# Kernel tuning notes

Hardware: AMD Instinct MI355X
Metric: run time of the kernel (lower is better)

## Reference

```python
import jax, jax.numpy as jnp
import numpy as np

P = 8192          # pool_size
D = 4096          # input_dim
B = 4             # batch
SPARSITY = 0.1
NC = int(P * P * SPARSITY)  # 6710886 COO nonzeros


def setup_inputs() -> dict:
    key = jax.random.key(0)
    ks = jax.random.split(key, 5)
    return {
        "x": jax.random.normal(ks[0], (B, D), dtype=jnp.float32),
        "W_proj": jax.random.normal(ks[1], (P, D), dtype=jnp.float32) / np.float32(np.sqrt(D)),
        "b_proj": jnp.zeros((P,), dtype=jnp.float32),
        "conn_values": jax.random.normal(ks[2], (NC,), dtype=jnp.float32) * 0.1,
        "sparse_state": jnp.zeros((P,), dtype=jnp.float32),
        "conn_rows": jax.random.randint(ks[3], (NC,), 0, P, dtype=jnp.int32),
        "conn_cols": jax.random.randint(ks[4], (NC,), 0, P, dtype=jnp.int32),
    }


def reference(x, W_proj, b_proj, conn_values, sparse_state, conn_rows, conn_cols):
    # input projection: [B, D] @ [D, P] -> [B, P]
    a = x @ W_proj.T + b_proj
    # quantile threshold over all elements of |a| (matches torch.quantile on full tensor)
    thr = jnp.quantile(jnp.abs(a), 1.0 - SPARSITY)
    mask = jnp.abs(a) > thr                     # [B, P]
    # decay old state, then overwrite active entries with row-0 activation
    a0, m0 = a[0], mask[0]                      # [P], [P]
    state = jnp.where(m0, a0, sparse_state * 0.9)
    # sparse COO matvec: recurrent[r] += v * state[c] for each nonzero (r, c, v)
    contrib = conn_values * state[conn_cols]    # [NC]
    recurrent = jax.ops.segment_sum(contrib, conn_rows, num_segments=P)
    # fused state update + exact GELU (torch nn.GELU default)
    new_state = jax.nn.gelu(state + 0.1 * recurrent, approximate=False)
    # BoundedAttractorState scalars
    active_count = m0.sum()
    mean_activity = jnp.where(
        active_count > 0,
        jnp.sum(jnp.where(m0, new_state, 0.0)) / jnp.maximum(active_count, 1).astype(new_state.dtype),
        0.0,
    )
    return new_state, active_count, mean_activity
```

## Files before the change

kernel.cpp:

```cpp
#include <hip/hip_runtime.h>
#include <math.h>

#define PP 8192
#define DD 4096
#define NTOT 32768
#define K_LOW 29490
#define NBINS 8192
#define SCALE 1048576.0f
#define INV_SCALE (1.0f / 1048576.0f)
#define MSCALE 262144.0f
#define INV_MSCALE (1.0f / 262144.0f)
#define LIST_CAP 3072

__device__ __forceinline__ float dot4(float4 w, float4 v) {
  return fmaf(w.x, v.x, fmaf(w.y, v.y, fmaf(w.z, v.z, w.w * v.w)));
}

__global__ __launch_bounds__(256, 4) void gemm_kernel(const float* __restrict__ x,
                                                      const float* __restrict__ W,
                                                      const float* __restrict__ bias,
                                                      float* __restrict__ a,
                                                      unsigned* __restrict__ hist,
                                                      int* __restrict__ rec,
                                                      int* __restrict__ acc) {
  if (blockIdx.x < 32) {
    hist[blockIdx.x * 256 + threadIdx.x] = 0u;
  } else if (blockIdx.x < 64) {
    rec[(blockIdx.x - 32) * 256 + threadIdx.x] = 0;
  } else if (blockIdx.x == 64 && threadIdx.x < 4) {
    acc[threadIdx.x] = 0;
  }
  const int wave = threadIdx.x >> 6;
  const int lane = threadIdx.x & 63;
  const int p0 = blockIdx.x * 8 + wave * 2;
  const float4* __restrict__ W0 = (const float4*)(W + (size_t)p0 * DD);
  const float4* __restrict__ W1 = W0 + (DD / 4);
  const float4* __restrict__ x4 = (const float4*)x;
  double a00 = 0.0, a01 = 0.0, a02 = 0.0, a03 = 0.0;
  double a10 = 0.0, a11 = 0.0, a12 = 0.0, a13 = 0.0;
  #pragma unroll 4
  for (int k = 0; k < 16; ++k) {
    const int i = lane + k * 64;
    float4 w0 = W0[i];
    float4 w1 = W1[i];
    float4 v0 = x4[i];
    float4 v1 = x4[1024 + i];
    float4 v2 = x4[2048 + i];
    float4 v3 = x4[3072 + i];
    a00 += (double)dot4(w0, v0);
    a01 += (double)dot4(w0, v1);
    a02 += (double)dot4(w0, v2);
    a03 += (double)dot4(w0, v3);
    a10 += (double)dot4(w1, v0);
    a11 += (double)dot4(w1, v1);
    a12 += (double)dot4(w1, v2);
    a13 += (double)dot4(w1, v3);
  }
  #pragma unroll
  for (int off = 32; off > 0; off >>= 1) {
    a00 += __shfl_down(a00, off);
    a01 += __shfl_down(a01, off);
    a02 += __shfl_down(a02, off);
    a03 += __shfl_down(a03, off);
    a10 += __shfl_down(a10, off);
    a11 += __shfl_down(a11, off);
    a12 += __shfl_down(a12, off);
    a13 += __shfl_down(a13, off);
  }
  if (lane == 0) {
    float b0 = bias[p0];
    float b1 = bias[p0 + 1];
    a[0 * PP + p0] = (float)a00 + b0;
    a[1 * PP + p0] = (float)a01 + b0;
    a[2 * PP + p0] = (float)a02 + b0;
    a[3 * PP + p0] = (float)a03 + b0;
    a[0 * PP + p0 + 1] = (float)a10 + b1;
    a[1 * PP + p0 + 1] = (float)a11 + b1;
    a[2 * PP + p0 + 1] = (float)a12 + b1;
    a[3 * PP + p0 + 1] = (float)a13 + b1;
  }
}

__global__ __launch_bounds__(1024) void hist_thr_kernel(const float* __restrict__ a,
                                                        unsigned* __restrict__ hist,
                                                        int* __restrict__ acc,
                                                        float* __restrict__ thr) {
  __shared__ union {
    unsigned h[NBINS];
    struct {
      unsigned scan[1024];
      unsigned list1[LIST_CAP];
      unsigned list2[LIST_CAP];
      unsigned n1, n2, b1, r1, b2, r2, vlo, vhi;
    } t;
  } sh;
  __shared__ int s_last;
  const int tid = threadIdx.x;

  #pragma unroll
  for (int j = 0; j < NBINS / 1024; ++j) sh.h[tid + j * 1024] = 0u;
  __syncthreads();
  const int base = blockIdx.x * 4096 + tid;
  #pragma unroll
  for (int k = 0; k < 4; ++k) {
    unsigned u = __float_as_uint(fabsf(a[base + k * 1024]));
    atomicAdd(&sh.h[u >> 18], 1u);
  }
  __syncthreads();
  #pragma unroll
  for (int j = 0; j < NBINS / 1024; ++j) {
    unsigned c = sh.h[tid + j * 1024];
    if (c) atomicAdd(&hist[tid + j * 1024], c);
  }

  __threadfence();
  __syncthreads();
  if (tid == 0) {
    unsigned d = atomicAdd((unsigned*)&acc[3], 1u);
    s_last = (d == 7u) ? 1 : 0;
  }
  __syncthreads();
  if (!s_last) return;
  __threadfence();

  const uint4* h4 = (const uint4*)hist;
  uint4 q0 = h4[tid * 2];
  uint4 q1 = h4[tid * 2 + 1];
  unsigned part = q0.x + q0.y + q0.z + q0.w + q1.x + q1.y + q1.z + q1.w;
  __syncthreads();
  sh.t.scan[tid] = part;
  if (tid == 0) { sh.t.n1 = 0; sh.t.n2 = 0; }
  __syncthreads();
  for (int off = 1; off < 1024; off <<= 1) {
    unsigned v = (tid >= off) ? sh.t.scan[tid - off] : 0u;
    __syncthreads();
    sh.t.scan[tid] += v;
    __syncthreads();
  }
  const unsigned incl = sh.t.scan[tid];
  const unsigned excl = incl - part;
  unsigned bins[8] = {q0.x, q0.y, q0.z, q0.w, q1.x, q1.y, q1.z, q1.w};
  if (excl <= (unsigned)K_LOW && (unsigned)K_LOW < incl) {
    unsigned r = (unsigned)K_LOW - excl, cum = 0;
    #pragma unroll
    for (int j = 0; j < 8; ++j) {
      if (cum + bins[j] > r) { sh.t.b1 = tid * 8 + j; sh.t.r1 = r - cum; break; }
      cum += bins[j];
    }
  }
  if (excl <= (unsigned)(K_LOW + 1) && (unsigned)(K_LOW + 1) < incl) {
    unsigned r = (unsigned)(K_LOW + 1) - excl, cum = 0;
    #pragma unroll
    for (int j = 0; j < 8; ++j) {
      if (cum + bins[j] > r) { sh.t.b2 = tid * 8 + j; sh.t.r2 = r - cum; break; }
      cum += bins[j];
    }
  }
  __syncthreads();
  const unsigned b1 = sh.t.b1, r1 = sh.t.r1, b2 = sh.t.b2, r2 = sh.t.r2;
  for (int i = tid; i < NTOT; i += 1024) {
    unsigned u = __float_as_uint(fabsf(a[i]));
    unsigned bk = u >> 18;
    if (bk == b1) {
      unsigned idx = atomicAdd(&sh.t.n1, 1u);
      if (idx < LIST_CAP) sh.t.list1[idx] = u;
    } else if (bk == b2) {
      unsigned idx = atomicAdd(&sh.t.n2, 1u);
      if (idx < LIST_CAP) sh.t.list2[idx] = u;
    }
  }
  __syncthreads();
  const unsigned m1 = min(sh.t.n1, (unsigned)LIST_CAP);
  const unsigned m2 = min(sh.t.n2, (unsigned)LIST_CAP);
  for (unsigned i = tid; i < m1; i += 1024) {
    unsigned ui = sh.t.list1[i];
    unsigned ltc = 0, eqb = 0;
    for (unsigned j = 0; j < m1; ++j) {
      unsigned uj = sh.t.list1[j];
      ltc += (uj < ui) ? 1u : 0u;
      eqb += ((uj == ui) && (j < i)) ? 1u : 0u;
    }
    unsigned rk = ltc + eqb;
    if (rk == r1) sh.t.vlo = ui;
    if (b2 == b1 && rk == r2) sh.t.vhi = ui;
  }
  if (b2 != b1) {
    for (unsigned i = tid; i < m2; i += 1024) {
      unsigned ui = sh.t.list2[i];
      unsigned ltc = 0, eqb = 0;
      for (unsigned j = 0; j < m2; ++j) {
        unsigned uj = sh.t.list2[j];
        ltc += (uj < ui) ? 1u : 0u;
        eqb += ((uj == ui) && (j < i)) ? 1u : 0u;
      }
      if (ltc + eqb == r2) sh.t.vhi = ui;
    }
  }
  __syncthreads();
  if (tid == 0) {
    double dlo = (double)__uint_as_float(sh.t.vlo);
    double dhi = (double)__uint_as_float(sh.t.vhi);
    double idx = 0.9 * (double)(NTOT - 1);
    double g = idx - floor(idx);
    thr[0] = (float)(dlo + g * (dhi - dlo));
  }
}

__global__ __launch_bounds__(1024) void spmv_kernel(const float* __restrict__ vals,
                                                    const int* __restrict__ rows,
                                                    const int* __restrict__ cols,
                                                    const float* __restrict__ a,
                                                    const float* __restrict__ thr,
                                                    const float* __restrict__ sstate,
                                                    int* __restrict__ rec,
                                                    int nc) {
  __shared__ float s_state[PP];
  __shared__ int s_rec[PP];
  const int tid = threadIdx.x;
  const float t = thr[0];
  for (int i = tid; i < PP; i += 1024) {
    float a0 = a[i];
    s_state[i] = (fabsf(a0) > t) ? a0 : 0.9f * sstate[i];
    s_rec[i] = 0;
  }
  __syncthreads();
  const int n4 = nc >> 2;
  const int stride = gridDim.x * 1024;
  const float4* __restrict__ v4 = (const float4*)vals;
  const int4* __restrict__ r4 = (const int4*)rows;
  const int4* __restrict__ c4 = (const int4*)cols;
  for (int i = blockIdx.x * 1024 + tid; i < n4; i += stride) {
    float4 v = v4[i];
    int4 r = r4[i];
    int4 c = c4[i];
    atomicAdd((unsigned*)&s_rec[r.x], (unsigned)__float2int_rn(v.x * s_state[c.x] * SCALE));
    atomicAdd((unsigned*)&s_rec[r.y], (unsigned)__float2int_rn(v.y * s_state[c.y] * SCALE));
    atomicAdd((unsigned*)&s_rec[r.z], (unsigned)__float2int_rn(v.z * s_state[c.z] * SCALE));
    atomicAdd((unsigned*)&s_rec[r.w], (unsigned)__float2int_rn(v.w * s_state[c.w] * SCALE));
  }
  if (blockIdx.x == 0 && tid < (nc - (n4 << 2))) {
    int i = (n4 << 2) + tid;
    atomicAdd((unsigned*)&s_rec[rows[i]],
              (unsigned)__float2int_rn(vals[i] * s_state[cols[i]] * SCALE));
  }
  __syncthreads();
  for (int i = tid; i < PP; i += 1024)
    atomicAdd((unsigned*)&rec[i], (unsigned)s_rec[i]);
}

__global__ __launch_bounds__(256) void finalize_kernel(const int* __restrict__ rec,
                                                       const float* __restrict__ a,
                                                       const float* __restrict__ thr,
                                                       const float* __restrict__ sstate,
                                                       float* __restrict__ out,
                                                       int* __restrict__ acc) {
  __shared__ float wsum[4];
  __shared__ unsigned wcnt[4];
  const int p = blockIdx.x * 256 + threadIdx.x;
  const float t = thr[0];
  float r = (float)rec[p] * INV_SCALE;
  float a0 = a[p];
  bool m = fabsf(a0) > t;
  float st = m ? a0 : 0.9f * sstate[p];
  float v = st + 0.1f * r;
  float ns = 0.5f * v * (1.0f + erff(v * 0.70710678118654752440f));
  out[p] = ns;
  float lsum = m ? ns : 0.0f;
  unsigned lcnt = m ? 1u : 0u;
  #pragma unroll
  for (int off = 32; off > 0; off >>= 1) {
    lsum += __shfl_down(lsum, off);
    lcnt += __shfl_down(lcnt, off);
  }
  const int lane = threadIdx.x & 63;
  const int wid = threadIdx.x >> 6;
  if (lane == 0) { wsum[wid] = lsum; wcnt[wid] = lcnt; }
  __syncthreads();
  if (threadIdx.x == 0) {
    float bsum = wsum[0] + wsum[1] + wsum[2] + wsum[3];
    unsigned bcnt = wcnt[0] + wcnt[1] + wcnt[2] + wcnt[3];
    atomicAdd((unsigned*)&acc[0], (unsigned)__float2int_rn(bsum * MSCALE));
    atomicAdd((unsigned*)&acc[1], bcnt);
    __threadfence();
    unsigned d = atomicAdd((unsigned*)&acc[2], 1u);
    if (d == (unsigned)(gridDim.x - 1)) {
      int sfix = (int)atomicAdd((unsigned*)&acc[0], 0u);
      int cnt = (int)atomicAdd((unsigned*)&acc[1], 0u);
      out[PP] = (float)cnt;
      out[PP + 1] = (cnt > 0) ? ((float)sfix * INV_MSCALE / (float)cnt) : 0.0f;
    }
  }
}

extern "C" void kernel_launch(void* const* d_in, const int* in_sizes, int n_in,
                              void* d_out, int out_size, void* d_ws, size_t ws_size,
                              hipStream_t stream) {
  const float* x      = (const float*)d_in[0];
  const float* W      = (const float*)d_in[1];
  const float* bias   = (const float*)d_in[2];
  const float* vals   = (const float*)d_in[3];
  const float* sstate = (const float*)d_in[4];
  const int*   rows   = (const int*)d_in[5];
  const int*   cols   = (const int*)d_in[6];
  const int    nc     = in_sizes[3];
  float* out = (float*)d_out;
  float* ws  = (float*)d_ws;

  float*    a    = ws;
  float*    thr  = ws + 32768;
  unsigned* hist = (unsigned*)(ws + 32784);
  int*      rec  = (int*)(ws + 32784 + NBINS);
  int*      acc  = (int*)(ws + 32784 + NBINS + PP);

  gemm_kernel<<<PP / 8, 256, 0, stream>>>(x, W, bias, a, hist, rec, acc);
  hist_thr_kernel<<<NTOT / 4096, 1024, 0, stream>>>(a, hist, acc, thr);
  spmv_kernel<<<256, 1024, 0, stream>>>(vals, rows, cols, a, thr, sstate, rec, nc);
  finalize_kernel<<<PP / 256, 256, 0, stream>>>(rec, a, thr, sstate, out, acc);
}
```

Baseline: 85.16 us.

## Replace global atomic merge of SpMV partials with per-block buffers reduced in finalize

Each SpMV block now writes its shared-memory accumulator to its own slice of a partials buffer with plain vector stores, instead of issuing 8192 global atomics per block. The finalize kernel sums the 256 partial rows per element, with 8 thread groups each covering 32 blocks, then reduces in shared memory and applies GELU and the mean/count accumulation. This removes atomic contention on the global recurrent array and the zeroing in the GEMM kernel. In exchange it adds about 8 MB of partial writes plus reads, and finalize now has only 32 active lanes per block doing the epilogue.

```diff
diff --git a/kernel.cpp b/kernel.cpp
--- a/kernel.cpp
+++ b/kernel.cpp
@@ -11,6 +11,7 @@
 #define MSCALE 262144.0f
 #define INV_MSCALE (1.0f / 262144.0f)
 #define LIST_CAP 3072
+#define NPB 256
 
 __device__ __forceinline__ float dot4(float4 w, float4 v) {
   return fmaf(w.x, v.x, fmaf(w.y, v.y, fmaf(w.z, v.z, w.w * v.w)));
@@ -21,13 +22,10 @@
                                                       const float* __restrict__ bias,
                                                       float* __restrict__ a,
                                                       unsigned* __restrict__ hist,
-                                                      int* __restrict__ rec,
                                                       int* __restrict__ acc) {
   if (blockIdx.x < 32) {
     hist[blockIdx.x * 256 + threadIdx.x] = 0u;
-  } else if (blockIdx.x < 64) {
-    rec[(blockIdx.x - 32) * 256 + threadIdx.x] = 0;
-  } else if (blockIdx.x == 64 && threadIdx.x < 4) {
+  } else if (blockIdx.x == 32 && threadIdx.x < 4) {
     acc[threadIdx.x] = 0;
   }
   const int wave = threadIdx.x >> 6;
@@ -212,7 +210,7 @@
                                                     const float* __restrict__ a,
                                                     const float* __restrict__ thr,
                                                     const float* __restrict__ sstate,
-                                                    int* __restrict__ rec,
+                                                    int* __restrict__ part,
                                                     int nc) {
   __shared__ float s_state[PP];
   __shared__ int s_rec[PP];
@@ -244,43 +242,54 @@
               (unsigned)__float2int_rn(vals[i] * s_state[cols[i]] * SCALE));
   }
   __syncthreads();
-  for (int i = tid; i < PP; i += 1024)
-    atomicAdd((unsigned*)&rec[i], (unsigned)s_rec[i]);
-}
-
-__global__ __launch_bounds__(256) void finalize_kernel(const int* __restrict__ rec,
+  int4* dst = (int4*)(part + (size_t)blockIdx.x * PP);
+  const int4* src = (const int4*)s_rec;
+  for (int i = tid; i < PP / 4; i += 1024) dst[i] = src[i];
+}
+
+__global__ __launch_bounds__(256) void finalize_kernel(const int* __restrict__ part,
                                                        const float* __restrict__ a,
                                                        const float* __restrict__ thr,
                                                        const float* __restrict__ sstate,
                                                        float* __restrict__ out,
                                                        int* __restrict__ acc) {
-  __shared__ float wsum[4];
-  __shared__ unsigned wcnt[4];
-  const int p = blockIdx.x * 256 + threadIdx.x;
+  __shared__ int s_red[32][9];
+  const int tid = threadIdx.x;
+  const int pl = tid & 31;
+  const int cls = tid >> 5;
+  const int p = blockIdx.x * 32 + pl;
+  int s = 0;
+  #pragma unroll 8
+  for (int it = 0; it < 32; ++it) {
+    s += part[(size_t)(it * 8 + cls) * PP + p];
+  }
+  s_red[pl][cls] = s;
+  __syncthreads();
   const float t = thr[0];
-  float r = (float)rec[p] * INV_SCALE;
-  float a0 = a[p];
-  bool m = fabsf(a0) > t;
-  float st = m ? a0 : 0.9f * sstate[p];
-  float v = st + 0.1f * r;
-  float ns = 0.5f * v * (1.0f + erff(v * 0.70710678118654752440f));
-  out[p] = ns;
-  float lsum = m ? ns : 0.0f;
-  unsigned lcnt = m ? 1u : 0u;
+  float lsum = 0.0f;
+  unsigned lcnt = 0;
+  if (tid < 32) {
+    int tot = 0;
+    #pragma unroll
+    for (int c = 0; c < 8; ++c) tot += s_red[tid][c];
+    float r = (float)tot * INV_SCALE;
+    float a0 = a[p];
+    bool m = fabsf(a0) > t;
+    float st = m ? a0 : 0.9f * sstate[p];
+    float v = st + 0.1f * r;
+    float ns = 0.5f * v * (1.0f + erff(v * 0.70710678118654752440f));
+    out[p] = ns;
+    lsum = m ? ns : 0.0f;
+    lcnt = m ? 1u : 0u;
+  }
   #pragma unroll
   for (int off = 32; off > 0; off >>= 1) {
     lsum += __shfl_down(lsum, off);
     lcnt += __shfl_down(lcnt, off);
   }
-  const int lane = threadIdx.x & 63;
-  const int wid = threadIdx.x >> 6;
-  if (lane == 0) { wsum[wid] = lsum; wcnt[wid] = lcnt; }
-  __syncthreads();
-  if (threadIdx.x == 0) {
-    float bsum = wsum[0] + wsum[1] + wsum[2] + wsum[3];
-    unsigned bcnt = wcnt[0] + wcnt[1] + wcnt[2] + wcnt[3];
-    atomicAdd((unsigned*)&acc[0], (unsigned)__float2int_rn(bsum * MSCALE));
-    atomicAdd((unsigned*)&acc[1], bcnt);
+  if (tid == 0) {
+    atomicAdd((unsigned*)&acc[0], (unsigned)__float2int_rn(lsum * MSCALE));
+    atomicAdd((unsigned*)&acc[1], lcnt);
     __threadfence();
     unsigned d = atomicAdd((unsigned*)&acc[2], 1u);
     if (d == (unsigned)(gridDim.x - 1)) {
@@ -309,11 +318,11 @@
   float*    a    = ws;
   float*    thr  = ws + 32768;
   unsigned* hist = (unsigned*)(ws + 32784);
-  int*      rec  = (int*)(ws + 32784 + NBINS);
-  int*      acc  = (int*)(ws + 32784 + NBINS + PP);
-
-  gemm_kernel<<<PP / 8, 256, 0, stream>>>(x, W, bias, a, hist, rec, acc);
+  int*      acc  = (int*)(ws + 32784 + NBINS);
+  int*      part = (int*)(ws + 32784 + NBINS + 16);
+
+  gemm_kernel<<<PP / 8, 256, 0, stream>>>(x, W, bias, a, hist, acc);
   hist_thr_kernel<<<NTOT / 4096, 1024, 0, stream>>>(a, hist, acc, thr);
-  spmv_kernel<<<256, 1024, 0, stream>>>(vals, rows, cols, a, thr, sstate, rec, nc);
-  finalize_kernel<<<PP / 256, 256, 0, stream>>>(rec, a, thr, sstate, out, acc);
-}
+  spmv_kernel<<<NPB, 1024, 0, stream>>>(vals, rows, cols, a, thr, sstate, part, nc);
+  finalize_kernel<<<PP / 32, 256, 0, stream>>>(part, a, thr, sstate, out, acc);
+}
```

Result: slower. 90.91 us (+6.7%).
